# Kernel optimization log

Hardware: AMD Instinct MI355X
Metric: run time of the kernel (lower is better)

## Reference

```python
import jax, jax.numpy as jnp
import numpy as np

N_EMBED = 8192
EMBED_DIM = 4
BETA = 0.25


def setup_inputs() -> dict:
    key = jax.random.key(0)
    k1, k2 = jax.random.split(key)
    z = jax.random.normal(k1, (8, EMBED_DIM, 64, 64), dtype=jnp.float32)
    # torch init: uniform(-1/n_embed, 1/n_embed)
    embed_w = jax.random.uniform(k2, (N_EMBED, EMBED_DIM), dtype=jnp.float32,
                                 minval=-1.0 / N_EMBED, maxval=1.0 / N_EMBED)
    return {"z": z, "embed_w": embed_w}


def reference(z, embed_w):
    # z: [B, C, H, W] -> [B, H, W, C]
    z_nhwc = jnp.transpose(z, (0, 2, 3, 1))
    z_flat = z_nhwc.reshape(-1, EMBED_DIM)  # [N, D]
    # squared L2 distances: ||z||^2 + ||e||^2 - 2 z e^T  -> [N, n_embed]
    d = (jnp.sum(z_flat * z_flat, axis=1, keepdims=True)
         + jnp.sum(embed_w * embed_w, axis=1)
         - 2.0 * z_flat @ embed_w.T)
    min_idx = jnp.argmin(d, axis=1)  # [N] int
    z_q = embed_w[min_idx].reshape(z_nhwc.shape)  # [B, H, W, C]
    sg = jax.lax.stop_gradient
    loss = (jnp.mean((sg(z_q) - z_nhwc) ** 2)
            + BETA * jnp.mean((z_q - sg(z_nhwc)) ** 2))
    # straight-through estimator
    z_q_ste = z_nhwc + sg(z_q - z_nhwc)
    z_q_out = jnp.transpose(z_q_ste, (0, 3, 1, 2))  # back to [B, C, H, W]
    return z_q_out, loss, min_idx
```

## Files before the change

kernel.cpp:

```cpp
#include <hip/hip_runtime.h>
#include <math.h>

typedef float v2f __attribute__((ext_vector_type(2)));

#define N_POINTS 32768
#define NUM_EMBED 8192
#define NPAIRS 4096
#define CH 64
#define CPC (NUM_EMBED / CH)
#define PAIRS (NPAIRS / CH)
#define PPT 4
#define RB 1024
#define RPB (RB / 64)
#define CSTRIDE 4096

__global__ void vq_prep_kernel(const float4* __restrict__ E, v2f* __restrict__ Epk) {
    int p = blockIdx.x * 256 + threadIdx.x;
    if (p < NPAIRS) {
        float4 a = E[2 * p];
        float4 b = E[2 * p + 1];
        Epk[4 * p + 0] = (v2f){a.x, b.x};
        Epk[4 * p + 1] = (v2f){a.y, b.y};
        Epk[4 * p + 2] = (v2f){a.z, b.z};
        Epk[4 * p + 3] = (v2f){a.w, b.w};
    }
}

__device__ __forceinline__ v2f pk_mul(v2f a, v2f b) {
    v2f d; asm("v_pk_mul_f32 %0, %1, %2" : "=v"(d) : "v"(a), "v"(b)); return d;
}
__device__ __forceinline__ v2f pk_fma(v2f a, v2f b, v2f c) {
    v2f d; asm("v_pk_fma_f32 %0, %1, %2, %3" : "=v"(d) : "v"(a), "v"(b), "v"(c)); return d;
}

__device__ __forceinline__ unsigned int fkey(float f) {
    unsigned int b = __float_as_uint(f);
    return b ^ (0x80000000u | (unsigned int)((int)b >> 31));
}

__global__ __launch_bounds__(256) void vq_filter_kernel(
        const float* __restrict__ z, const v2f* __restrict__ Epk,
        float* __restrict__ cmax) {
    __shared__ alignas(16) v2f sE[PAIRS * 4];

    const int c = blockIdx.y;
    if (threadIdx.x < PAIRS * 2) {
        ((float4*)sE)[threadIdx.x] =
            ((const float4*)(Epk + (size_t)c * PAIRS * 4))[threadIdx.x];
    }

    const int n0 = blockIdx.x * (256 * PPT) + threadIdx.x;

    v2f zv[PPT][4];
    #pragma unroll
    for (int p = 0; p < PPT; ++p) {
        int n = n0 + p * 256;
        int b = n >> 12, hw = n & 4095;
        const float* zp = z + b * 16384 + hw;
        zv[p][0] = (v2f){zp[0], zp[0]};
        zv[p][1] = (v2f){zp[CSTRIDE], zp[CSTRIDE]};
        zv[p][2] = (v2f){zp[2 * CSTRIDE], zp[2 * CSTRIDE]};
        zv[p][3] = (v2f){zp[3 * CSTRIDE], zp[3 * CSTRIDE]};
    }

    __syncthreads();

    float run[PPT];
    #pragma unroll
    for (int p = 0; p < PPT; ++p) run[p] = -__builtin_inff();

    const float4* sE4 = (const float4*)sE;
    #pragma unroll 4
    for (int t = 0; t < PAIRS; ++t) {
        float4 E01 = sE4[2 * t];
        float4 E23 = sE4[2 * t + 1];
        v2f e0 = {E01.x, E01.y};
        v2f e1 = {E01.z, E01.w};
        v2f e2 = {E23.x, E23.y};
        v2f e3 = {E23.z, E23.w};
        #pragma unroll
        for (int p = 0; p < PPT; ++p) {
            v2f dot = pk_mul(zv[p][0], e0);
            dot = pk_fma(zv[p][1], e1, dot);
            dot = pk_fma(zv[p][2], e2, dot);
            dot = pk_fma(zv[p][3], e3, dot);
            run[p] = fmaxf(fmaxf(dot.x, dot.y), run[p]);
        }
    }

    #pragma unroll
    for (int p = 0; p < PPT; ++p)
        cmax[(size_t)c * N_POINTS + n0 + p * 256] = run[p];
}

__global__ __launch_bounds__(RB) void vq_resolve_kernel(
        const float* __restrict__ z, const float4* __restrict__ E,
        const float* __restrict__ cmax,
        float* __restrict__ out, double* __restrict__ partial) {
    __shared__ float sCm[CH][RPB + 1];
    __shared__ double sdata[RPB];
    const int lane = threadIdx.x & 63;
    const int wid = threadIdx.x >> 6;
    const int n0 = blockIdx.x * RPB;
    const int n = n0 + wid;

    {
        int t = threadIdx.x;
        sCm[t >> 4][t & 15] = cmax[(size_t)(t >> 4) * N_POINTS + n0 + (t & 15)];
    }

    const int b = n >> 12;
    const int hw = n & 4095;
    const float* zp = z + b * 16384 + hw;
    float z0 = zp[0];
    float z1 = zp[CSTRIDE];
    float z2 = zp[2 * CSTRIDE];
    float z3 = zp[3 * CSTRIDE];
    float zz = __fmul_rn(z0, z0);
    zz = __fadd_rn(zz, __fmul_rn(z1, z1));
    zz = __fadd_rn(zz, __fmul_rn(z2, z2));
    zz = __fadd_rn(zz, __fmul_rn(z3, z3));

    __syncthreads();

    float cm = sCm[lane][wid];
    float gmax = cm;
    #pragma unroll
    for (int off = 32; off; off >>= 1)
        gmax = fmaxf(gmax, __shfl_xor(gmax, off));

    float u = __fmul_rn(__fadd_rn(zz, 0.01f), 2.38418579e-07f);
    float thr = __fsub_rn(gmax, __fadd_rn(__fadd_rn(u, u), 1e-7f));
    unsigned long long mask = __ballot(cm >= thr);

    unsigned long long bkey = ~0ull;
    while (mask) {
        int c = __builtin_ctzll(mask);
        mask &= mask - 1ull;
        int j0 = c * CPC + lane;
        #pragma unroll
        for (int h = 0; h < 2; ++h) {
            int j = j0 + h * 64;
            float4 e = E[j];
            float ee = __fmul_rn(e.x, e.x);
            ee = __fadd_rn(ee, __fmul_rn(e.y, e.y));
            ee = __fadd_rn(ee, __fmul_rn(e.z, e.z));
            ee = __fadd_rn(ee, __fmul_rn(e.w, e.w));
            float dot = __fmul_rn(z0, e.x);
            dot = __fmaf_rn(z1, e.y, dot);
            dot = __fmaf_rn(z2, e.z, dot);
            dot = __fmaf_rn(z3, e.w, dot);
            float d = __fmaf_rn(-2.0f, dot, __fadd_rn(zz, ee));
            unsigned long long key =
                ((unsigned long long)fkey(d) << 32) | (unsigned int)j;
            bkey = key < bkey ? key : bkey;
        }
    }
    #pragma unroll
    for (int off = 32; off; off >>= 1) {
        unsigned long long o = __shfl_xor(bkey, off);
        bkey = o < bkey ? o : bkey;
    }
    int besti = (int)(unsigned int)(bkey & 0xFFFFFFFFull);

    if (lane == 0) {
        float4 e = E[besti];
        float* op = out + b * 16384 + hw;
        float t0 = __fsub_rn(e.x, z0);
        float t1 = __fsub_rn(e.y, z1);
        float t2 = __fsub_rn(e.z, z2);
        float t3 = __fsub_rn(e.w, z3);
        op[0]           = __fadd_rn(z0, t0);
        op[CSTRIDE]     = __fadd_rn(z1, t1);
        op[2 * CSTRIDE] = __fadd_rn(z2, t2);
        op[3 * CSTRIDE] = __fadd_rn(z3, t3);
        out[131073 + n] = (float)besti;
        double ds = (double)__fmul_rn(t0, t0) + (double)__fmul_rn(t1, t1)
                  + (double)__fmul_rn(t2, t2) + (double)__fmul_rn(t3, t3);
        sdata[wid] = ds;
    }
    __syncthreads();
    if (threadIdx.x == 0) {
        double s = 0.0;
        #pragma unroll
        for (int w = 0; w < RPB; ++w) s += sdata[w];
        partial[blockIdx.x] = s;
    }
}

__global__ void vq_loss_kernel(const double* __restrict__ partial, float* __restrict__ out) {
    __shared__ double sdata[256];
    int t = threadIdx.x;
    double s = 0.0;
    for (int i = t; i < 2048; i += 256) s += partial[i];
    sdata[t] = s;
    __syncthreads();
    #pragma unroll
    for (int st = 128; st > 0; st >>= 1) {
        if (t < st) sdata[t] += sdata[t + st];
        __syncthreads();
    }
    if (t == 0) {
        float m = (float)(sdata[0] / 131072.0);
        out[131072] = __fadd_rn(m, __fmul_rn(0.25f, m));
    }
}

extern "C" void kernel_launch(void* const* d_in, const int* in_sizes, int n_in,
                              void* d_out, int out_size, void* d_ws, size_t ws_size,
                              hipStream_t stream) {
    const float* z = (const float*)d_in[0];
    const float4* E = (const float4*)d_in[1];
    float* out = (float*)d_out;

    char* ws = (char*)d_ws;
    v2f* Epk = (v2f*)ws;
    float* cmaxb = (float*)(ws + 131072);
    double* partial = (double*)(ws + 131072 + (size_t)CH * N_POINTS * 4);

    vq_prep_kernel<<<NPAIRS / 256, 256, 0, stream>>>(E, Epk);
    vq_filter_kernel<<<dim3(N_POINTS / (256 * PPT), CH), 256, 0, stream>>>(z, Epk, cmaxb);
    vq_resolve_kernel<<<N_POINTS / RPB, RB, 0, stream>>>(z, E, cmaxb, out, partial);
    vq_loss_kernel<<<1, 256, 0, stream>>>(partial, out);
}
```

Before: 53.03 us.

## Compute coarse filter distances with bf16 MFMA and widen resolve slack

Replaces the packed-FP32 VALU filter with a bf16 MFMA 16x16x32 filter. z and the codebook are first packed to bf16 by a new pack kernel, and each wave computes per-chunk max dot products for 16 points against all codes. The resolve kernel's candidate threshold gains an L1-proportional slack to absorb bf16 rounding error, so exact fp32 resolution remains correct. The MFMA only uses 4 of its 32 K slots and 16 lanes carry operands, so utilisation is low. The wider slack may admit more candidate chunks in resolve.

Result: slower. 70.60 us (+33.1%).

```diff
diff --git a/kernel.cpp b/kernel.cpp
--- a/kernel.cpp
+++ b/kernel.cpp
@@ -1,36 +1,27 @@
 #include <hip/hip_runtime.h>
+#include <hip/hip_bf16.h>
 #include <math.h>
 
 typedef float v2f __attribute__((ext_vector_type(2)));
+typedef __attribute__((ext_vector_type(8))) short bf16x8;
+typedef __attribute__((ext_vector_type(4))) float f32x4;
+typedef __attribute__((ext_vector_type(4))) int i32x4;
 
 #define N_POINTS 32768
 #define NUM_EMBED 8192
-#define NPAIRS 4096
 #define CH 64
 #define CPC (NUM_EMBED / CH)
-#define PAIRS (NPAIRS / CH)
-#define PPT 4
 #define RB 1024
 #define RPB (RB / 64)
+#define FWAVES 4
 #define CSTRIDE 4096
 
-__global__ void vq_prep_kernel(const float4* __restrict__ E, v2f* __restrict__ Epk) {
-    int p = blockIdx.x * 256 + threadIdx.x;
-    if (p < NPAIRS) {
-        float4 a = E[2 * p];
-        float4 b = E[2 * p + 1];
-        Epk[4 * p + 0] = (v2f){a.x, b.x};
-        Epk[4 * p + 1] = (v2f){a.y, b.y};
-        Epk[4 * p + 2] = (v2f){a.z, b.z};
-        Epk[4 * p + 3] = (v2f){a.w, b.w};
-    }
-}
-
-__device__ __forceinline__ v2f pk_mul(v2f a, v2f b) {
-    v2f d; asm("v_pk_mul_f32 %0, %1, %2" : "=v"(d) : "v"(a), "v"(b)); return d;
-}
-__device__ __forceinline__ v2f pk_fma(v2f a, v2f b, v2f c) {
-    v2f d; asm("v_pk_fma_f32 %0, %1, %2, %3" : "=v"(d) : "v"(a), "v"(b), "v"(c)); return d;
+__device__ __forceinline__ unsigned int bfr(float f) {
+    __hip_bfloat16 h = __float2bfloat16(f);
+    return (unsigned int)*reinterpret_cast<unsigned short*>(&h);
+}
+__device__ __forceinline__ uint2 pack4(float a, float b, float c, float d) {
+    return make_uint2(bfr(a) | (bfr(b) << 16), bfr(c) | (bfr(d) << 16));
 }
 
 __device__ __forceinline__ unsigned int fkey(float f) {
@@ -38,59 +29,49 @@
     return b ^ (0x80000000u | (unsigned int)((int)b >> 31));
 }
 
-__global__ __launch_bounds__(256) void vq_filter_kernel(
-        const float* __restrict__ z, const v2f* __restrict__ Epk,
+__global__ void vq_pack_kernel(const float* __restrict__ z, const float4* __restrict__ E,
+                               uint2* __restrict__ zbf, uint2* __restrict__ ebf) {
+    int i = blockIdx.x * 256 + threadIdx.x;
+    if (i < N_POINTS) {
+        int b = i >> 12, hw = i & 4095;
+        const float* zp = z + b * 16384 + hw;
+        zbf[i] = pack4(zp[0], zp[CSTRIDE], zp[2 * CSTRIDE], zp[3 * CSTRIDE]);
+    }
+    if (i < NUM_EMBED) {
+        float4 e = E[i];
+        ebf[i] = pack4(e.x, e.y, e.z, e.w);
+    }
+}
+
+__global__ __launch_bounds__(256) void vq_mfma_filter(
+        const uint2* __restrict__ zbf, const uint2* __restrict__ ebf,
         float* __restrict__ cmax) {
-    __shared__ alignas(16) v2f sE[PAIRS * 4];
-
-    const int c = blockIdx.y;
-    if (threadIdx.x < PAIRS * 2) {
-        ((float4*)sE)[threadIdx.x] =
-            ((const float4*)(Epk + (size_t)c * PAIRS * 4))[threadIdx.x];
-    }
-
-    const int n0 = blockIdx.x * (256 * PPT) + threadIdx.x;
-
-    v2f zv[PPT][4];
-    #pragma unroll
-    for (int p = 0; p < PPT; ++p) {
-        int n = n0 + p * 256;
-        int b = n >> 12, hw = n & 4095;
-        const float* zp = z + b * 16384 + hw;
-        zv[p][0] = (v2f){zp[0], zp[0]};
-        zv[p][1] = (v2f){zp[CSTRIDE], zp[CSTRIDE]};
-        zv[p][2] = (v2f){zp[2 * CSTRIDE], zp[2 * CSTRIDE]};
-        zv[p][3] = (v2f){zp[3 * CSTRIDE], zp[3 * CSTRIDE]};
-    }
-
-    __syncthreads();
-
-    float run[PPT];
-    #pragma unroll
-    for (int p = 0; p < PPT; ++p) run[p] = -__builtin_inff();
-
-    const float4* sE4 = (const float4*)sE;
-    #pragma unroll 4
-    for (int t = 0; t < PAIRS; ++t) {
-        float4 E01 = sE4[2 * t];
-        float4 E23 = sE4[2 * t + 1];
-        v2f e0 = {E01.x, E01.y};
-        v2f e1 = {E01.z, E01.w};
-        v2f e2 = {E23.x, E23.y};
-        v2f e3 = {E23.z, E23.w};
+    const int lane = threadIdx.x & 63;
+    const int wid = threadIdx.x >> 6;
+    const int wv = blockIdx.x * FWAVES + wid;
+    const int n0 = wv * 16;
+
+    const bool lo = lane < 16;
+    uint2 zl = zbf[n0 + (lane & 15)];
+    i32x4 bi = { lo ? (int)zl.x : 0, lo ? (int)zl.y : 0, 0, 0 };
+    bf16x8 bfrag = *(bf16x8*)&bi;
+    const f32x4 zero4 = {0.f, 0.f, 0.f, 0.f};
+
+    for (int c = 0; c < CH; ++c) {
+        float rm = -__builtin_inff();
         #pragma unroll
-        for (int p = 0; p < PPT; ++p) {
-            v2f dot = pk_mul(zv[p][0], e0);
-            dot = pk_fma(zv[p][1], e1, dot);
-            dot = pk_fma(zv[p][2], e2, dot);
-            dot = pk_fma(zv[p][3], e3, dot);
-            run[p] = fmaxf(fmaxf(dot.x, dot.y), run[p]);
+        for (int t = 0; t < 8; ++t) {
+            int j0 = (c * 8 + t) * 16;
+            uint2 el = ebf[j0 + (lane & 15)];
+            i32x4 ai = { lo ? (int)el.x : 0, lo ? (int)el.y : 0, 0, 0 };
+            bf16x8 afrag = *(bf16x8*)&ai;
+            f32x4 d = __builtin_amdgcn_mfma_f32_16x16x32_bf16(afrag, bfrag, zero4, 0, 0, 0);
+            rm = fmaxf(rm, fmaxf(fmaxf(d[0], d[1]), fmaxf(d[2], d[3])));
         }
-    }
-
-    #pragma unroll
-    for (int p = 0; p < PPT; ++p)
-        cmax[(size_t)c * N_POINTS + n0 + p * 256] = run[p];
+        rm = fmaxf(rm, __shfl_xor(rm, 16));
+        rm = fmaxf(rm, __shfl_xor(rm, 32));
+        if (lo) cmax[(size_t)c * N_POINTS + n0 + lane] = rm;
+    }
 }
 
 __global__ __launch_bounds__(RB) void vq_resolve_kernel(
@@ -130,7 +111,9 @@
         gmax = fmaxf(gmax, __shfl_xor(gmax, off));
 
     float u = __fmul_rn(__fadd_rn(zz, 0.01f), 2.38418579e-07f);
-    float thr = __fsub_rn(gmax, __fadd_rn(__fadd_rn(u, u), 1e-7f));
+    float L1 = __fadd_rn(__fadd_rn(fabsf(z0), fabsf(z1)), __fadd_rn(fabsf(z2), fabsf(z3)));
+    float slack = __fadd_rn(__fadd_rn(u, u), __fmaf_rn(L1, 2.0e-6f, 2.0e-7f));
+    float thr = __fsub_rn(gmax, slack);
     unsigned long long mask = __ballot(cm >= thr);
 
     unsigned long long bkey = ~0ull;
@@ -214,12 +197,13 @@
     float* out = (float*)d_out;
 
     char* ws = (char*)d_ws;
-    v2f* Epk = (v2f*)ws;
-    float* cmaxb = (float*)(ws + 131072);
-    double* partial = (double*)(ws + 131072 + (size_t)CH * N_POINTS * 4);
-
-    vq_prep_kernel<<<NPAIRS / 256, 256, 0, stream>>>(E, Epk);
-    vq_filter_kernel<<<dim3(N_POINTS / (256 * PPT), CH), 256, 0, stream>>>(z, Epk, cmaxb);
+    uint2* zbf = (uint2*)ws;
+    uint2* ebf = (uint2*)(ws + 262144);
+    float* cmaxb = (float*)(ws + 262144 + 65536);
+    double* partial = (double*)(ws + 262144 + 65536 + (size_t)CH * N_POINTS * 4);
+
+    vq_pack_kernel<<<N_POINTS / 256, 256, 0, stream>>>(z, E, zbf, ebf);
+    vq_mfma_filter<<<(N_POINTS / 16) / FWAVES, 256, 0, stream>>>(zbf, ebf, cmaxb);
     vq_resolve_kernel<<<N_POINTS / RPB, RB, 0, stream>>>(z, E, cmaxb, out, partial);
     vq_loss_kernel<<<1, 256, 0, stream>>>(partial, out);
 }
```
